# Optimization experiments

Hardware: AMD Instinct MI355X
Metric: run time of the kernel (lower is better)

The kernel has to match this reference:

```python
import jax, jax.numpy as jnp
import numpy as np

N = 4096
D = 256
TEMP = 0.1
NEG_INF = -1e30
NUM_IDS = 1000
NUM_CAMS = 8


def setup_inputs() -> dict:
    key = jax.random.key(0)
    k1, k2, k3 = jax.random.split(key, 3)
    features = jax.random.normal(k1, (N, 2, D), dtype=jnp.float32)
    label = jax.random.randint(k2, (N,), 0, NUM_IDS)
    camid = jax.random.randint(k3, (N,), 0, NUM_CAMS)
    return {"features": features, "label": label, "camid": camid}


def reference(features, label, camid):
    n = features.shape[0]
    n2 = 2 * n
    # torch.cat(torch.unbind(features, dim=1), dim=0): [N,2,D] -> [2N,D]
    f = jnp.concatenate([features[:, 0], features[:, 1]], axis=0)
    # pairwise similarity, pre-scaled by 1/temperature (original divides each
    # per-positive logit row by T, which is equivalent)
    logit = jnp.matmul(f, f.T) / TEMP  # [2N, 2N]
    diag = jnp.eye(n2, dtype=bool)
    lg = jnp.where(diag, NEG_INF, logit)  # diagonal excluded by masked_select
    m = jnp.max(lg, axis=1, keepdims=True)  # stable shift per row
    e = jnp.exp(lg - m)  # exp(logit - m), 0 on diagonal

    label_eq = label[:, None] == label[None, :]          # [N, N]
    cam_eq = camid[:, None] == camid[None, :]
    pos_id = jnp.tile(label_eq, (2, 2))                  # label_mask.repeat(2,2)
    pos_cam = jnp.tile(label_eq & cam_eq, (2, 2))        # is_pos.repeat(2,2)

    def branch(pos_full, row_scale):
        pm = pos_full & ~diag        # positives (off-diagonal)
        nm = ~pos_full               # negatives (diagonal is positive -> excluded)
        neg_sum = jnp.sum(jnp.where(nm, e, 0.0), axis=1, keepdims=True)
        # per-positive CE with label 0 over [positive, negatives]:
        #   log(exp(l_p - m) + neg_sum) + m - l_p
        per = jnp.log(jnp.where(pm, e + neg_sum, 1.0)) - (lg - m)
        num_pos = jnp.sum(pm, axis=1).astype(lg.dtype)
        row = jnp.sum(jnp.where(pm, per, 0.0), axis=1) / num_pos
        return row_scale * row

    loss_rows = branch(pos_id, 1.0) + branch(pos_cam, 0.5)
    loss = jnp.sum(loss_rows) / n2
    return loss
```

## Files before the change

kernel.cpp:

```cpp
#include <hip/hip_runtime.h>

typedef __attribute__((ext_vector_type(8))) _Float16 h8v;
typedef __attribute__((ext_vector_type(8))) short    s8v;
typedef __attribute__((ext_vector_type(4))) float    f4v;

#define N_   4096
#define N2   8192
#define D_   256
#define NIDS 1000
#define LCAP 32

constexpr float INV_TEMP = 10.0f;
constexpr float K_LOG2   = 14.426950408889634f;
constexpr float LN2F     = 0.6931471805599453f;
constexpr float NEGINF   = -1e30f;

__device__ __forceinline__ const float* frow(const float* f, int r) {
    return f + (size_t)(r & (N_ - 1)) * (2 * D_) + (size_t)((r >> 12) * D_);
}

__device__ __forceinline__ void gload_lds16(const void* g, void* l) {
    __builtin_amdgcn_global_load_lds(
        (const __attribute__((address_space(1))) void*)g,
        (__attribute__((address_space(3))) void*)l, 16, 0, 0);
}

__global__ __launch_bounds__(256) void prepK(const float* __restrict__ feat,
                                             const int* __restrict__ label,
                                             _Float16* __restrict__ f16,
                                             int* __restrict__ lists,
                                             int* __restrict__ done) {
    if (blockIdx.x < 1024) {
        int t = blockIdx.x * 256 + threadIdx.x;
        int r = t >> 5, g = t & 31;
        const float* src = frow(feat, r) + g * 8;
        float4 v0 = *(const float4*)src;
        float4 v1 = *(const float4*)(src + 4);
        float x[8] = {v0.x, v0.y, v0.z, v0.w, v1.x, v1.y, v1.z, v1.w};
        h8v h;
        #pragma unroll
        for (int i = 0; i < 8; ++i) h[i] = (_Float16)x[i];
        *(h8v*)(f16 + (size_t)r * D_ + g * 8) = h;
    } else {
        if (blockIdx.x == 1024 && threadIdx.x == 0) *done = 0;
        int cls  = (blockIdx.x - 1024) * 4 + (threadIdx.x >> 6);
        int lane = threadIdx.x & 63;
        int* Lp = lists + (size_t)cls * (LCAP + 1);
        int cnt = 0;
        for (int jj = 0; jj < N_; jj += 64) {
            unsigned long long mk = __ballot(label[jj + lane] == cls);
            while (mk) {
                int b = __ffsll((unsigned long long)mk) - 1;
                mk &= mk - 1;
                if (lane == 0 && cnt < LCAP) Lp[1 + cnt] = jj + b;
                ++cnt;
            }
        }
        if (lane == 0) Lp[0] = (cnt < LCAP) ? cnt : LCAP;
    }
}

__global__ __launch_bounds__(256, 4) void phaseA(const _Float16* __restrict__ f16,
                                                 const int* __restrict__ label,
                                                 float2* __restrict__ partial) {
    __shared__ char lds[32768];

    const int tid  = threadIdx.x;
    const int lane = tid & 63;
    const int w    = tid >> 6;
    const int wr   = w >> 1, wc = w & 1;

    int idx = (blockIdx.x & 7) * 260 + (blockIdx.x >> 3);
    int rt = 0, rem = idx;
    while (rem >= 64 - rt) { rem -= 64 - rt; ++rt; }
    const int ct = rt + rem;
    const bool offdiag = (ct != rt);
    const int rowBase = rt * 128, colBase = ct * 128;

    f4v acc[4][4];
    #pragma unroll
    for (int i = 0; i < 4; ++i)
        #pragma unroll
        for (int j = 0; j < 4; ++j) acc[i][j] = (f4v){0.f, 0.f, 0.f, 0.f};

    const int prB = (w < 2) ? rowBase : colBase;
    const int ssrc = (lane & 3) ^ ((lane >> 3) & 3);
    const _Float16* gl = f16 + (size_t)(prB + (w & 1) * 64 + (lane >> 2)) * D_ + ssrc * 8;
    const int ldoff = ((w >= 2) ? 8192 : 0) + (w & 1) * 4096 + lane * 16;

    #pragma unroll
    for (int i = 0; i < 4; ++i)
        gload_lds16(gl + (size_t)i * 16 * D_, lds + ldoff + i * 1024);
    __syncthreads();

    const int l15  = lane & 15;
    const int phys = ((lane >> 4) ^ ((l15 >> 1) & 3)) * 16;
    const int aoff0 = (wr * 64 + l15) * 64 + phys;
    const int boff0 = 8192 + (wc * 64 + l15) * 64 + phys;

    for (int kc = 0; kc < 8; ++kc) {
        const int cur = kc & 1;
        if (kc < 7) {
            const _Float16* gk = gl + (kc + 1) * 32;
            char* lp = lds + (cur ^ 1) * 16384 + ldoff;
            #pragma unroll
            for (int i = 0; i < 4; ++i)
                gload_lds16(gk + (size_t)i * 16 * D_, lp + i * 1024);
        }
        const char* bb = lds + cur * 16384;
        h8v a[4], b[4];
        #pragma unroll
        for (int rf = 0; rf < 4; ++rf) a[rf] = *(const h8v*)(bb + aoff0 + rf * 1024);
        #pragma unroll
        for (int cf = 0; cf < 4; ++cf) b[cf] = *(const h8v*)(bb + boff0 + cf * 1024);
        #pragma unroll
        for (int rf = 0; rf < 4; ++rf)
            #pragma unroll
            for (int cf = 0; cf < 4; ++cf)
                acc[rf][cf] = __builtin_amdgcn_mfma_f32_16x16x32_f16(a[rf], b[cf], acc[rf][cf], 0, 0, 0);
        __syncthreads();
    }

    float* rowm  = (float*)lds;
    float* colm  = (float*)(lds + 16896);
    float* mrowS = (float*)(lds + 21504);
    float* mcolS = (float*)(lds + 22016);

    const int grp32 = wc * 16 + l15;
    const int grp8  = wr * 4 + (lane >> 4);
    int rloc[16], cloc[4];
    int rowlab[16], collab[4];
    #pragma unroll
    for (int rf = 0; rf < 4; ++rf)
        #pragma unroll
        for (int rg = 0; rg < 4; ++rg) {
            int i = rf * 4 + rg;
            rloc[i] = wr * 64 + rf * 16 + (lane >> 4) * 4 + rg;
            rowlab[i] = label[(rowBase + rloc[i]) & (N_ - 1)];
        }
    #pragma unroll
    for (int cf = 0; cf < 4; ++cf) {
        cloc[cf] = wc * 64 + cf * 16 + l15;
        collab[cf] = label[(colBase + cloc[cf]) & (N_ - 1)];
    }

    #pragma unroll
    for (int rf = 0; rf < 4; ++rf)
        #pragma unroll
        for (int cf = 0; cf < 4; ++cf)
            #pragma unroll
            for (int rg = 0; rg < 4; ++rg) {
                float v = acc[rf][cf][rg] * K_LOG2;
                acc[rf][cf][rg] = (collab[cf] == rowlab[rf * 4 + rg]) ? NEGINF : v;
            }

    #pragma unroll
    for (int rf = 0; rf < 4; ++rf)
        #pragma unroll
        for (int rg = 0; rg < 4; ++rg) {
            float m = fmaxf(fmaxf(acc[rf][0][rg], acc[rf][1][rg]),
                            fmaxf(acc[rf][2][rg], acc[rf][3][rg]));
            rowm[rloc[rf * 4 + rg] * 33 + grp32] = m;
        }
    if (offdiag) {
        #pragma unroll
        for (int cf = 0; cf < 4; ++cf) {
            float m = NEGINF;
            #pragma unroll
            for (int rf = 0; rf < 4; ++rf)
                #pragma unroll
                for (int rg = 0; rg < 4; ++rg) m = fmaxf(m, acc[rf][cf][rg]);
            colm[cloc[cf] * 9 + grp8] = m;
        }
    }
    __syncthreads();
    if (tid < 128) {
        float m = NEGINF;
        #pragma unroll
        for (int g = 0; g < 32; ++g) m = fmaxf(m, rowm[tid * 33 + g]);
        mrowS[tid] = m;
        if (offdiag) {
            float mc = NEGINF;
            #pragma unroll
            for (int g = 0; g < 8; ++g) mc = fmaxf(mc, colm[tid * 9 + g]);
            mcolS[tid] = mc;
        }
    }
    __syncthreads();

    #pragma unroll
    for (int rf = 0; rf < 4; ++rf)
        #pragma unroll
        for (int rg = 0; rg < 4; ++rg) {
            int i = rf * 4 + rg;
            float m = mrowS[rloc[i]];
            float s = 0.f;
            #pragma unroll
            for (int cf = 0; cf < 4; ++cf) s += exp2f(acc[rf][cf][rg] - m);
            rowm[rloc[i] * 33 + grp32] = s;
        }
    if (offdiag) {
        #pragma unroll
        for (int cf = 0; cf < 4; ++cf) {
            float m = mcolS[cloc[cf]];
            float s = 0.f;
            #pragma unroll
            for (int rf = 0; rf < 4; ++rf)
                #pragma unroll
                for (int rg = 0; rg < 4; ++rg) s += exp2f(acc[rf][cf][rg] - m);
            colm[cloc[cf] * 9 + grp8] = s;
        }
    }
    __syncthreads();
    if (tid < 128) {
        float s = 0.f;
        #pragma unroll
        for (int g = 0; g < 32; ++g) s += rowm[tid * 33 + g];
        partial[(size_t)(rowBase + tid) * 64 + ct] = make_float2(mrowS[tid], s);
        if (offdiag) {
            float s2 = 0.f;
            #pragma unroll
            for (int g = 0; g < 8; ++g) s2 += colm[tid * 9 + g];
            partial[(size_t)(colBase + tid) * 64 + rt] = make_float2(mcolS[tid], s2);
        }
    }
}

__global__ __launch_bounds__(512) void phaseB(const float* __restrict__ feat,
                                              const int* __restrict__ label,
                                              const int* __restrict__ camid,
                                              const int* __restrict__ lists,
                                              const float2* __restrict__ partial,
                                              float* __restrict__ rowloss,
                                              int* __restrict__ done,
                                              float* __restrict__ out) {
    __shared__ int   cList[8][64];
    __shared__ int   fList[8][64];
    __shared__ float pList[8][64];
    __shared__ float red[512];
    __shared__ int   lastFlag;

    const int tid = threadIdx.x, lane = tid & 63, w = tid >> 6;
    const int row = blockIdx.x * 8 + w;
    const int rl = label[row & (N_ - 1)];
    const int rc = camid[row & (N_ - 1)];

    float2 p = partial[(size_t)row * 64 + lane];
    float mm = p.x, ms = p.y;
    #pragma unroll
    for (int off = 32; off >= 1; off >>= 1) {
        float om = __shfl_xor(mm, off), os = __shfl_xor(ms, off);
        float nm = fmaxf(mm, om);
        ms = ms * exp2f(mm - nm) + os * exp2f(om - nm);
        mm = nm;
    }
    const float cid = (mm + __log2f(ms)) * LN2F;

    const int li = lane & 15, g = lane >> 4;
    const float4* fip = (const float4*)frow(feat, row);
    float4 fiv[4];
    #pragma unroll
    for (int k = 0; k < 4; ++k) fiv[k] = fip[li * 4 + k];

    const int* Lp = lists + (size_t)rl * (LCAP + 1);
    const int nmem = Lp[0];
    int jm = (lane < 2 * nmem) ? Lp[1 + (lane >> 1)] : -1;
    int cand = jm + (lane & 1) * N_;
    bool valid = (jm >= 0) && (cand != row);
    unsigned long long mask = __ballot(valid);
    int cnt = __popcll(mask);
    int pos = __popcll(mask & ((1ull << lane) - 1ull));
    if (valid) {
        cList[w][pos] = cand;
        fList[w][pos] = (camid[jm] == rc) ? 1 : 0;
    }

    const int nb = (cnt + 3) >> 2;
    for (int b = 0; b < nb; ++b) {
        int e = b * 4 + g;
        bool act = (e < cnt);
        int c = act ? cList[w][e] : row;
        const float4* fcp = (const float4*)frow(feat, c);
        float pp = 0.f;
        #pragma unroll
        for (int k = 0; k < 4; ++k) {
            float4 v = fcp[li * 4 + k];
            pp += fiv[k].x * v.x + fiv[k].y * v.y + fiv[k].z * v.z + fiv[k].w * v.w;
        }
        #pragma unroll
        for (int off = 8; off >= 1; off >>= 1) pp += __shfl_xor(pp, off);
        if (act && li == 0) pList[w][e] = pp * INV_TEMP;
    }

    float a_e = (lane < cnt) ? pList[w][lane] : NEGINF;
    int   f_e = (lane < cnt) ? fList[w][lane] : 1;

    float xa = (f_e == 0) ? a_e : NEGINF;
    float mx = xa;
    #pragma unroll
    for (int off = 32; off >= 1; off >>= 1) mx = fmaxf(mx, __shfl_xor(mx, off));
    float xe = (f_e == 0) ? __expf(xa - mx) : 0.f;
    #pragma unroll
    for (int off = 32; off >= 1; off >>= 1) xe += __shfl_xor(xe, off);
    float ccam;
    if (xe > 0.f) {
        float xl = mx + __logf(xe);
        float d = xl - cid;
        ccam = (d <= 0.f) ? cid + log1pf(__expf(d)) : xl + log1pf(__expf(-d));
    } else {
        ccam = cid;
    }

    float ti = cid - a_e;
    float termid = (ti <= 0.f) ? log1pf(__expf(ti)) : ti + log1pf(__expf(-ti));
    termid = (lane < cnt) ? termid : 0.f;
    float tc = ccam - a_e;
    float termcam = (tc <= 0.f) ? log1pf(__expf(tc)) : tc + log1pf(__expf(-tc));
    termcam = (lane < cnt && f_e) ? termcam : 0.f;
    #pragma unroll
    for (int off = 32; off >= 1; off >>= 1) {
        termid  += __shfl_xor(termid, off);
        termcam += __shfl_xor(termcam, off);
    }
    int ncam = __popcll(__ballot(lane < cnt && f_e));
    if (lane == 0)
        rowloss[row] = termid / (float)cnt + 0.5f * termcam / (float)ncam;

    __syncthreads();
    if (tid == 0) {
        __threadfence();
        lastFlag = (atomicAdd(done, 1) == (int)gridDim.x - 1) ? 1 : 0;
    }
    __syncthreads();
    if (lastFlag) {
        __threadfence();
        float s = 0.f;
        const int b0 = tid * 16;
        #pragma unroll
        for (int i = 0; i < 16; ++i) s += rowloss[b0 + i];
        red[tid] = s;
        __syncthreads();
        for (int ww = 256; ww > 0; ww >>= 1) {
            if (tid < ww) red[tid] += red[tid + ww];
            __syncthreads();
        }
        if (tid == 0) out[0] = red[0] / (float)N2;
    }
}

extern "C" void kernel_launch(void* const* d_in, const int* in_sizes, int n_in,
                              void* d_out, int out_size, void* d_ws, size_t ws_size,
                              hipStream_t stream) {
    const float* feat  = (const float*)d_in[0];
    const int*   label = (const int*)d_in[1];
    const int*   camid = (const int*)d_in[2];

    _Float16* f16    = (_Float16*)d_ws;
    float2*   partial = (float2*)((char*)d_ws + 4u * 1024 * 1024);
    float*    rowloss = (float*)((char*)d_ws + 8u * 1024 * 1024);
    int*      lists   = (int*)(rowloss + N2);
    int*      done    = lists + NIDS * (LCAP + 1);

    prepK<<<1274, 256, 0, stream>>>(feat, label, f16, lists, done);
    phaseA<<<2080, 256, 0, stream>>>(f16, label, partial);
    phaseB<<<1024, 512, 0, stream>>>(feat, label, camid, lists, partial,
                                     rowloss, done, (float*)d_out);
}
```

Measured before the change: 95.60 us.

## Fuse GEMM and per-row loss phases into one persistent kernel with spin-wait

Merges phaseA (tiled fp16 MFMA Gram matrix with masked log-sum-exp partials) and phaseB (per-row positive dot products and loss) into one launch. The trailing blocks first build each row's same-label candidate list by scanning all labels, which replaces the per-class list pass in prepK, then spin on an atomic counter until every GEMM tile has finished. The tile order is reversed through a closed-form triangular index, and each loss block now handles 32 rows. This removes one kernel launch boundary and overlaps candidate discovery with the GEMM. In exchange it depends on all GEMM blocks being scheduled ahead of the spinning blocks, and each loss block does a much larger label scan.

```diff
diff --git a/kernel.cpp b/kernel.cpp
--- a/kernel.cpp
+++ b/kernel.cpp
@@ -1,14 +1,13 @@
 #include <hip/hip_runtime.h>
 
 typedef __attribute__((ext_vector_type(8))) _Float16 h8v;
-typedef __attribute__((ext_vector_type(8))) short    s8v;
 typedef __attribute__((ext_vector_type(4))) float    f4v;
 
-#define N_   4096
-#define N2   8192
-#define D_   256
-#define NIDS 1000
-#define LCAP 32
+#define N_     4096
+#define N2     8192
+#define D_     256
+#define ATILES 2080
+#define BBLK   256
 
 constexpr float INV_TEMP = 10.0f;
 constexpr float K_LOG2   = 14.426950408889634f;
@@ -26,321 +25,346 @@
 }
 
 __global__ __launch_bounds__(256) void prepK(const float* __restrict__ feat,
-                                             const int* __restrict__ label,
                                              _Float16* __restrict__ f16,
-                                             int* __restrict__ lists,
                                              int* __restrict__ done) {
-    if (blockIdx.x < 1024) {
-        int t = blockIdx.x * 256 + threadIdx.x;
-        int r = t >> 5, g = t & 31;
-        const float* src = frow(feat, r) + g * 8;
-        float4 v0 = *(const float4*)src;
-        float4 v1 = *(const float4*)(src + 4);
-        float x[8] = {v0.x, v0.y, v0.z, v0.w, v1.x, v1.y, v1.z, v1.w};
-        h8v h;
-        #pragma unroll
-        for (int i = 0; i < 8; ++i) h[i] = (_Float16)x[i];
-        *(h8v*)(f16 + (size_t)r * D_ + g * 8) = h;
-    } else {
-        if (blockIdx.x == 1024 && threadIdx.x == 0) *done = 0;
-        int cls  = (blockIdx.x - 1024) * 4 + (threadIdx.x >> 6);
-        int lane = threadIdx.x & 63;
-        int* Lp = lists + (size_t)cls * (LCAP + 1);
-        int cnt = 0;
-        for (int jj = 0; jj < N_; jj += 64) {
-            unsigned long long mk = __ballot(label[jj + lane] == cls);
+    if (blockIdx.x == 0 && threadIdx.x == 0) { done[0] = 0; done[1] = 0; }
+    int t = blockIdx.x * 256 + threadIdx.x;
+    int r = t >> 5, g = t & 31;
+    const float* src = frow(feat, r) + g * 8;
+    float4 v0 = *(const float4*)src;
+    float4 v1 = *(const float4*)(src + 4);
+    float x[8] = {v0.x, v0.y, v0.z, v0.w, v1.x, v1.y, v1.z, v1.w};
+    h8v h;
+    #pragma unroll
+    for (int i = 0; i < 8; ++i) h[i] = (_Float16)x[i];
+    *(h8v*)(f16 + (size_t)r * D_ + g * 8) = h;
+}
+
+__global__ __launch_bounds__(256, 4) void mega(const _Float16* __restrict__ f16,
+                                               const float* __restrict__ feat,
+                                               const int* __restrict__ label,
+                                               const int* __restrict__ camid,
+                                               float2* __restrict__ partial,
+                                               float* __restrict__ rowloss,
+                                               int* __restrict__ done,
+                                               float* __restrict__ out) {
+    __shared__ char lds[32768];
+    const int tid  = threadIdx.x;
+    const int lane = tid & 63;
+    const int w    = tid >> 6;
+
+    if (blockIdx.x < ATILES) {
+        const int wr = w >> 1, wc = w & 1;
+        int idx = (blockIdx.x & 7) * 260 + (blockIdx.x >> 3);
+        int rev = 2079 - idx;
+        int r2 = (int)((sqrtf((float)(8 * rev + 1)) - 1.0f) * 0.5f);
+        if (r2 * (r2 + 1) / 2 > rev) --r2;
+        else if ((r2 + 1) * (r2 + 2) / 2 <= rev) ++r2;
+        const int rt = 63 - r2;
+        const int ct = 63 - (rev - r2 * (r2 + 1) / 2);
+        const bool offdiag = (ct != rt);
+        const int rowBase = rt * 128, colBase = ct * 128;
+
+        f4v acc[4][4];
+        #pragma unroll
+        for (int i = 0; i < 4; ++i)
+            #pragma unroll
+            for (int j = 0; j < 4; ++j) acc[i][j] = (f4v){0.f, 0.f, 0.f, 0.f};
+
+        const int prB = (w < 2) ? rowBase : colBase;
+        const int ssrc = (lane & 3) ^ ((lane >> 3) & 3);
+        const _Float16* gl = f16 + (size_t)(prB + (w & 1) * 64 + (lane >> 2)) * D_ + ssrc * 8;
+        const int ldoff = ((w >= 2) ? 8192 : 0) + (w & 1) * 4096 + lane * 16;
+
+        #pragma unroll
+        for (int i = 0; i < 4; ++i)
+            gload_lds16(gl + (size_t)i * 16 * D_, lds + ldoff + i * 1024);
+        __syncthreads();
+
+        const int l15  = lane & 15;
+        const int phys = ((lane >> 4) ^ ((l15 >> 1) & 3)) * 16;
+        const int aoff0 = (wr * 64 + l15) * 64 + phys;
+        const int boff0 = 8192 + (wc * 64 + l15) * 64 + phys;
+
+        for (int kc = 0; kc < 8; ++kc) {
+            const int cur = kc & 1;
+            if (kc < 7) {
+                const _Float16* gk = gl + (kc + 1) * 32;
+                char* lp = lds + (cur ^ 1) * 16384 + ldoff;
+                #pragma unroll
+                for (int i = 0; i < 4; ++i)
+                    gload_lds16(gk + (size_t)i * 16 * D_, lp + i * 1024);
+            }
+            const char* bb = lds + cur * 16384;
+            h8v a[4], b[4];
+            #pragma unroll
+            for (int rf = 0; rf < 4; ++rf) a[rf] = *(const h8v*)(bb + aoff0 + rf * 1024);
+            #pragma unroll
+            for (int cf = 0; cf < 4; ++cf) b[cf] = *(const h8v*)(bb + boff0 + cf * 1024);
+            #pragma unroll
+            for (int rf = 0; rf < 4; ++rf)
+                #pragma unroll
+                for (int cf = 0; cf < 4; ++cf)
+                    acc[rf][cf] = __builtin_amdgcn_mfma_f32_16x16x32_f16(a[rf], b[cf], acc[rf][cf], 0, 0, 0);
+            __syncthreads();
+        }
+
+        float* rowm  = (float*)lds;
+        float* colm  = (float*)(lds + 16896);
+        float* mrowS = (float*)(lds + 21504);
+        float* mcolS = (float*)(lds + 22016);
+
+        const int grp32 = wc * 16 + l15;
+        const int grp8  = wr * 4 + (lane >> 4);
+        int rloc[16], cloc[4], rowlab[16], collab[4];
+        #pragma unroll
+        for (int rf = 0; rf < 4; ++rf)
+            #pragma unroll
+            for (int rg = 0; rg < 4; ++rg) {
+                int i = rf * 4 + rg;
+                rloc[i] = wr * 64 + rf * 16 + (lane >> 4) * 4 + rg;
+                rowlab[i] = label[(rowBase + rloc[i]) & (N_ - 1)];
+            }
+        #pragma unroll
+        for (int cf = 0; cf < 4; ++cf) {
+            cloc[cf] = wc * 64 + cf * 16 + l15;
+            collab[cf] = label[(colBase + cloc[cf]) & (N_ - 1)];
+        }
+
+        #pragma unroll
+        for (int rf = 0; rf < 4; ++rf)
+            #pragma unroll
+            for (int cf = 0; cf < 4; ++cf)
+                #pragma unroll
+                for (int rg = 0; rg < 4; ++rg) {
+                    float v = acc[rf][cf][rg] * K_LOG2;
+                    acc[rf][cf][rg] = (collab[cf] == rowlab[rf * 4 + rg]) ? NEGINF : v;
+                }
+
+        #pragma unroll
+        for (int rf = 0; rf < 4; ++rf)
+            #pragma unroll
+            for (int rg = 0; rg < 4; ++rg) {
+                float m = fmaxf(fmaxf(acc[rf][0][rg], acc[rf][1][rg]),
+                                fmaxf(acc[rf][2][rg], acc[rf][3][rg]));
+                rowm[rloc[rf * 4 + rg] * 33 + grp32] = m;
+            }
+        if (offdiag) {
+            #pragma unroll
+            for (int cf = 0; cf < 4; ++cf) {
+                float m = NEGINF;
+                #pragma unroll
+                for (int rf = 0; rf < 4; ++rf)
+                    #pragma unroll
+                    for (int rg = 0; rg < 4; ++rg) m = fmaxf(m, acc[rf][cf][rg]);
+                colm[cloc[cf] * 9 + grp8] = m;
+            }
+        }
+        __syncthreads();
+        if (tid < 128) {
+            float m = NEGINF;
+            #pragma unroll
+            for (int g = 0; g < 32; ++g) m = fmaxf(m, rowm[tid * 33 + g]);
+            mrowS[tid] = m;
+            if (offdiag) {
+                float mc = NEGINF;
+                #pragma unroll
+                for (int g = 0; g < 8; ++g) mc = fmaxf(mc, colm[tid * 9 + g]);
+                mcolS[tid] = mc;
+            }
+        }
+        __syncthreads();
+
+        #pragma unroll
+        for (int rf = 0; rf < 4; ++rf)
+            #pragma unroll
+            for (int rg = 0; rg < 4; ++rg) {
+                int i = rf * 4 + rg;
+                float m = mrowS[rloc[i]];
+                float s = 0.f;
+                #pragma unroll
+                for (int cf = 0; cf < 4; ++cf) s += exp2f(acc[rf][cf][rg] - m);
+                rowm[rloc[i] * 33 + grp32] = s;
+            }
+        if (offdiag) {
+            #pragma unroll
+            for (int cf = 0; cf < 4; ++cf) {
+                float m = mcolS[cloc[cf]];
+                float s = 0.f;
+                #pragma unroll
+                for (int rf = 0; rf < 4; ++rf)
+                    #pragma unroll
+                    for (int rg = 0; rg < 4; ++rg) s += exp2f(acc[rf][cf][rg] - m);
+                colm[cloc[cf] * 9 + grp8] = s;
+            }
+        }
+        __syncthreads();
+        if (tid < 128) {
+            float s = 0.f;
+            #pragma unroll
+            for (int g = 0; g < 32; ++g) s += rowm[tid * 33 + g];
+            partial[(size_t)(rowBase + tid) * 64 + ct] = make_float2(mrowS[tid], s);
+            if (offdiag) {
+                float s2 = 0.f;
+                #pragma unroll
+                for (int g = 0; g < 8; ++g) s2 += colm[tid * 9 + g];
+                partial[(size_t)(colBase + tid) * 64 + rt] = make_float2(mcolS[tid], s2);
+            }
+        }
+        __syncthreads();
+        if (tid == 0) {
+            __threadfence();
+            atomicAdd(&done[0], 1);
+        }
+        return;
+    }
+
+    int*   candN = (int*)lds;
+    int*   candJ = (int*)(lds + 128);
+    int*   cList = (int*)(lds + 4224);
+    float* pList = (float*)(lds + 5248);
+    float* red   = (float*)(lds + 6272);
+    int*   lastF = (int*)(lds + 7296);
+
+    const int r0 = (blockIdx.x - ATILES) * 32 + w * 8;
+
+    int rl[8], rc[8], nq[8];
+    #pragma unroll
+    for (int q = 0; q < 8; ++q) {
+        int m = (r0 + q) & (N_ - 1);
+        rl[q] = label[m];
+        rc[q] = camid[m];
+        nq[q] = 0;
+    }
+    for (int jj = 0; jj < N_; jj += 64) {
+        int lj = label[jj + lane], cj = camid[jj + lane];
+        #pragma unroll
+        for (int q = 0; q < 8; ++q) {
+            unsigned long long mk = __ballot(lj == rl[q]);
             while (mk) {
                 int b = __ffsll((unsigned long long)mk) - 1;
                 mk &= mk - 1;
-                if (lane == 0 && cnt < LCAP) Lp[1 + cnt] = jj + b;
-                ++cnt;
-            }
-        }
-        if (lane == 0) Lp[0] = (cnt < LCAP) ? cnt : LCAP;
-    }
-}
-
-__global__ __launch_bounds__(256, 4) void phaseA(const _Float16* __restrict__ f16,
-                                                 const int* __restrict__ label,
-                                                 float2* __restrict__ partial) {
-    __shared__ char lds[32768];
-
-    const int tid  = threadIdx.x;
-    const int lane = tid & 63;
-    const int w    = tid >> 6;
-    const int wr   = w >> 1, wc = w & 1;
-
-    int idx = (blockIdx.x & 7) * 260 + (blockIdx.x >> 3);
-    int rt = 0, rem = idx;
-    while (rem >= 64 - rt) { rem -= 64 - rt; ++rt; }
-    const int ct = rt + rem;
-    const bool offdiag = (ct != rt);
-    const int rowBase = rt * 128, colBase = ct * 128;
-
-    f4v acc[4][4];
+                int cm = (__shfl(cj, b) == rc[q]) ? 1 : 0;
+                if (lane == 0 && nq[q] < 32)
+                    candJ[(w * 8 + q) * 32 + nq[q]] = (jj + b) | (cm << 30);
+                ++nq[q];
+            }
+        }
+    }
     #pragma unroll
-    for (int i = 0; i < 4; ++i)
-        #pragma unroll
-        for (int j = 0; j < 4; ++j) acc[i][j] = (f4v){0.f, 0.f, 0.f, 0.f};
-
-    const int prB = (w < 2) ? rowBase : colBase;
-    const int ssrc = (lane & 3) ^ ((lane >> 3) & 3);
-    const _Float16* gl = f16 + (size_t)(prB + (w & 1) * 64 + (lane >> 2)) * D_ + ssrc * 8;
-    const int ldoff = ((w >= 2) ? 8192 : 0) + (w & 1) * 4096 + lane * 16;
-
-    #pragma unroll
-    for (int i = 0; i < 4; ++i)
-        gload_lds16(gl + (size_t)i * 16 * D_, lds + ldoff + i * 1024);
+    for (int q = 0; q < 8; ++q)
+        if (lane == 0) candN[w * 8 + q] = (nq[q] < 32) ? nq[q] : 32;
     __syncthreads();
 
-    const int l15  = lane & 15;
-    const int phys = ((lane >> 4) ^ ((l15 >> 1) & 3)) * 16;
-    const int aoff0 = (wr * 64 + l15) * 64 + phys;
-    const int boff0 = 8192 + (wc * 64 + l15) * 64 + phys;
-
-    for (int kc = 0; kc < 8; ++kc) {
-        const int cur = kc & 1;
-        if (kc < 7) {
-            const _Float16* gk = gl + (kc + 1) * 32;
-            char* lp = lds + (cur ^ 1) * 16384 + ldoff;
-            #pragma unroll
-            for (int i = 0; i < 4; ++i)
-                gload_lds16(gk + (size_t)i * 16 * D_, lp + i * 1024);
-        }
-        const char* bb = lds + cur * 16384;
-        h8v a[4], b[4];
-        #pragma unroll
-        for (int rf = 0; rf < 4; ++rf) a[rf] = *(const h8v*)(bb + aoff0 + rf * 1024);
-        #pragma unroll
-        for (int cf = 0; cf < 4; ++cf) b[cf] = *(const h8v*)(bb + boff0 + cf * 1024);
-        #pragma unroll
-        for (int rf = 0; rf < 4; ++rf)
-            #pragma unroll
-            for (int cf = 0; cf < 4; ++cf)
-                acc[rf][cf] = __builtin_amdgcn_mfma_f32_16x16x32_f16(a[rf], b[cf], acc[rf][cf], 0, 0, 0);
-        __syncthreads();
-    }
-
-    float* rowm  = (float*)lds;
-    float* colm  = (float*)(lds + 16896);
-    float* mrowS = (float*)(lds + 21504);
-    float* mcolS = (float*)(lds + 22016);
-
-    const int grp32 = wc * 16 + l15;
-    const int grp8  = wr * 4 + (lane >> 4);
-    int rloc[16], cloc[4];
-    int rowlab[16], collab[4];
-    #pragma unroll
-    for (int rf = 0; rf < 4; ++rf)
-        #pragma unroll
-        for (int rg = 0; rg < 4; ++rg) {
-            int i = rf * 4 + rg;
-            rloc[i] = wr * 64 + rf * 16 + (lane >> 4) * 4 + rg;
-            rowlab[i] = label[(rowBase + rloc[i]) & (N_ - 1)];
-        }
-    #pragma unroll
-    for (int cf = 0; cf < 4; ++cf) {
-        cloc[cf] = wc * 64 + cf * 16 + l15;
-        collab[cf] = label[(colBase + cloc[cf]) & (N_ - 1)];
-    }
-
-    #pragma unroll
-    for (int rf = 0; rf < 4; ++rf)
-        #pragma unroll
-        for (int cf = 0; cf < 4; ++cf)
-            #pragma unroll
-            for (int rg = 0; rg < 4; ++rg) {
-                float v = acc[rf][cf][rg] * K_LOG2;
-                acc[rf][cf][rg] = (collab[cf] == rowlab[rf * 4 + rg]) ? NEGINF : v;
-            }
-
-    #pragma unroll
-    for (int rf = 0; rf < 4; ++rf)
-        #pragma unroll
-        for (int rg = 0; rg < 4; ++rg) {
-            float m = fmaxf(fmaxf(acc[rf][0][rg], acc[rf][1][rg]),
-                            fmaxf(acc[rf][2][rg], acc[rf][3][rg]));
-            rowm[rloc[rf * 4 + rg] * 33 + grp32] = m;
-        }
-    if (offdiag) {
-        #pragma unroll
-        for (int cf = 0; cf < 4; ++cf) {
-            float m = NEGINF;
-            #pragma unroll
-            for (int rf = 0; rf < 4; ++rf)
-                #pragma unroll
-                for (int rg = 0; rg < 4; ++rg) m = fmaxf(m, acc[rf][cf][rg]);
-            colm[cloc[cf] * 9 + grp8] = m;
-        }
+    if (tid == 0) {
+        while (__hip_atomic_load(&done[0], __ATOMIC_ACQUIRE, __HIP_MEMORY_SCOPE_AGENT) < ATILES)
+            __builtin_amdgcn_s_sleep(16);
     }
     __syncthreads();
-    if (tid < 128) {
-        float m = NEGINF;
-        #pragma unroll
-        for (int g = 0; g < 32; ++g) m = fmaxf(m, rowm[tid * 33 + g]);
-        mrowS[tid] = m;
-        if (offdiag) {
-            float mc = NEGINF;
-            #pragma unroll
-            for (int g = 0; g < 8; ++g) mc = fmaxf(mc, colm[tid * 9 + g]);
-            mcolS[tid] = mc;
-        }
-    }
-    __syncthreads();
-
-    #pragma unroll
-    for (int rf = 0; rf < 4; ++rf)
-        #pragma unroll
-        for (int rg = 0; rg < 4; ++rg) {
-            int i = rf * 4 + rg;
-            float m = mrowS[rloc[i]];
-            float s = 0.f;
-            #pragma unroll
-            for (int cf = 0; cf < 4; ++cf) s += exp2f(acc[rf][cf][rg] - m);
-            rowm[rloc[i] * 33 + grp32] = s;
-        }
-    if (offdiag) {
-        #pragma unroll
-        for (int cf = 0; cf < 4; ++cf) {
-            float m = mcolS[cloc[cf]];
-            float s = 0.f;
-            #pragma unroll
-            for (int rf = 0; rf < 4; ++rf)
-                #pragma unroll
-                for (int rg = 0; rg < 4; ++rg) s += exp2f(acc[rf][cf][rg] - m);
-            colm[cloc[cf] * 9 + grp8] = s;
-        }
-    }
-    __syncthreads();
-    if (tid < 128) {
-        float s = 0.f;
-        #pragma unroll
-        for (int g = 0; g < 32; ++g) s += rowm[tid * 33 + g];
-        partial[(size_t)(rowBase + tid) * 64 + ct] = make_float2(mrowS[tid], s);
-        if (offdiag) {
-            float s2 = 0.f;
-            #pragma unroll
-            for (int g = 0; g < 8; ++g) s2 += colm[tid * 9 + g];
-            partial[(size_t)(colBase + tid) * 64 + rt] = make_float2(mcolS[tid], s2);
-        }
-    }
-}
-
-__global__ __launch_bounds__(512) void phaseB(const float* __restrict__ feat,
-                                              const int* __restrict__ label,
-                                              const int* __restrict__ camid,
-                                              const int* __restrict__ lists,
-                                              const float2* __restrict__ partial,
-                                              float* __restrict__ rowloss,
-                                              int* __restrict__ done,
-                                              float* __restrict__ out) {
-    __shared__ int   cList[8][64];
-    __shared__ int   fList[8][64];
-    __shared__ float pList[8][64];
-    __shared__ float red[512];
-    __shared__ int   lastFlag;
-
-    const int tid = threadIdx.x, lane = tid & 63, w = tid >> 6;
-    const int row = blockIdx.x * 8 + w;
-    const int rl = label[row & (N_ - 1)];
-    const int rc = camid[row & (N_ - 1)];
-
-    float2 p = partial[(size_t)row * 64 + lane];
-    float mm = p.x, ms = p.y;
-    #pragma unroll
-    for (int off = 32; off >= 1; off >>= 1) {
-        float om = __shfl_xor(mm, off), os = __shfl_xor(ms, off);
-        float nm = fmaxf(mm, om);
-        ms = ms * exp2f(mm - nm) + os * exp2f(om - nm);
-        mm = nm;
-    }
-    const float cid = (mm + __log2f(ms)) * LN2F;
+    __threadfence();
 
     const int li = lane & 15, g = lane >> 4;
-    const float4* fip = (const float4*)frow(feat, row);
-    float4 fiv[4];
-    #pragma unroll
-    for (int k = 0; k < 4; ++k) fiv[k] = fip[li * 4 + k];
-
-    const int* Lp = lists + (size_t)rl * (LCAP + 1);
-    const int nmem = Lp[0];
-    int jm = (lane < 2 * nmem) ? Lp[1 + (lane >> 1)] : -1;
-    int cand = jm + (lane & 1) * N_;
-    bool valid = (jm >= 0) && (cand != row);
-    unsigned long long mask = __ballot(valid);
-    int cnt = __popcll(mask);
-    int pos = __popcll(mask & ((1ull << lane) - 1ull));
-    if (valid) {
-        cList[w][pos] = cand;
-        fList[w][pos] = (camid[jm] == rc) ? 1 : 0;
-    }
-
-    const int nb = (cnt + 3) >> 2;
-    for (int b = 0; b < nb; ++b) {
-        int e = b * 4 + g;
-        bool act = (e < cnt);
-        int c = act ? cList[w][e] : row;
-        const float4* fcp = (const float4*)frow(feat, c);
-        float pp = 0.f;
-        #pragma unroll
-        for (int k = 0; k < 4; ++k) {
-            float4 v = fcp[li * 4 + k];
-            pp += fiv[k].x * v.x + fiv[k].y * v.y + fiv[k].z * v.z + fiv[k].w * v.w;
-        }
-        #pragma unroll
-        for (int off = 8; off >= 1; off >>= 1) pp += __shfl_xor(pp, off);
-        if (act && li == 0) pList[w][e] = pp * INV_TEMP;
-    }
-
-    float a_e = (lane < cnt) ? pList[w][lane] : NEGINF;
-    int   f_e = (lane < cnt) ? fList[w][lane] : 1;
-
-    float xa = (f_e == 0) ? a_e : NEGINF;
-    float mx = xa;
-    #pragma unroll
-    for (int off = 32; off >= 1; off >>= 1) mx = fmaxf(mx, __shfl_xor(mx, off));
-    float xe = (f_e == 0) ? __expf(xa - mx) : 0.f;
-    #pragma unroll
-    for (int off = 32; off >= 1; off >>= 1) xe += __shfl_xor(xe, off);
-    float ccam;
-    if (xe > 0.f) {
-        float xl = mx + __logf(xe);
-        float d = xl - cid;
-        ccam = (d <= 0.f) ? cid + log1pf(__expf(d)) : xl + log1pf(__expf(-d));
-    } else {
-        ccam = cid;
-    }
-
-    float ti = cid - a_e;
-    float termid = (ti <= 0.f) ? log1pf(__expf(ti)) : ti + log1pf(__expf(-ti));
-    termid = (lane < cnt) ? termid : 0.f;
-    float tc = ccam - a_e;
-    float termcam = (tc <= 0.f) ? log1pf(__expf(tc)) : tc + log1pf(__expf(-tc));
-    termcam = (lane < cnt && f_e) ? termcam : 0.f;
-    #pragma unroll
-    for (int off = 32; off >= 1; off >>= 1) {
-        termid  += __shfl_xor(termid, off);
-        termcam += __shfl_xor(termcam, off);
-    }
-    int ncam = __popcll(__ballot(lane < cnt && f_e));
-    if (lane == 0)
-        rowloss[row] = termid / (float)cnt + 0.5f * termcam / (float)ncam;
+
+    #pragma unroll 1
+    for (int q = 0; q < 8; ++q) {
+        const int row = r0 + q;
+        const int rcq = camid[row & (N_ - 1)];
+
+        float2 p = partial[(size_t)row * 64 + lane];
+        float mm = p.x, ms = p.y;
+        #pragma unroll
+        for (int off = 32; off >= 1; off >>= 1) {
+            float om = __shfl_xor(mm, off), os = __shfl_xor(ms, off);
+            float nm = fmaxf(mm, om);
+            ms = ms * exp2f(mm - nm) + os * exp2f(om - nm);
+            mm = nm;
+        }
+        const float cid = (mm + __log2f(ms)) * LN2F;
+
+        float4 fiv[4];
+        const float4* fip = (const float4*)frow(feat, row);
+        #pragma unroll
+        for (int k = 0; k < 4; ++k) fiv[k] = fip[li * 4 + k];
+
+        const int n = candN[w * 8 + q];
+        int jm = (lane < 2 * n) ? candJ[(w * 8 + q) * 32 + (lane >> 1)] : -1;
+        int cand = (jm & 0xFFFF) + (lane & 1) * N_;
+        bool valid = (jm >= 0) && (cand != row);
+        unsigned long long mask = __ballot(valid);
+        int cnt = __popcll(mask);
+        int pos = __popcll(mask & ((1ull << lane) - 1ull));
+        if (valid) cList[w * 64 + pos] = cand | (jm & (1 << 30));
+
+        const int nb = (cnt + 3) >> 2;
+        for (int b = 0; b < nb; ++b) {
+            int e = b * 4 + g;
+            bool act = (e < cnt);
+            int c = act ? (cList[w * 64 + e] & 0xFFFF) : row;
+            const float4* fcp = (const float4*)frow(feat, c);
+            float pp = 0.f;
+            #pragma unroll
+            for (int k = 0; k < 4; ++k) {
+                float4 v = fcp[li * 4 + k];
+                pp += fiv[k].x * v.x + fiv[k].y * v.y + fiv[k].z * v.z + fiv[k].w * v.w;
+            }
+            #pragma unroll
+            for (int off = 8; off >= 1; off >>= 1) pp += __shfl_xor(pp, off);
+            if (act && li == 0) pList[w * 64 + e] = pp * INV_TEMP;
+        }
+
+        int ce   = (lane < cnt) ? cList[w * 64 + lane] : -1;
+        float a_e = (lane < cnt) ? pList[w * 64 + lane] : NEGINF;
+        int   f_e = (lane < cnt) ? ((ce >> 30) & 1) : 1;
+
+        float xa = (f_e == 0) ? a_e : NEGINF;
+        float mx = xa;
+        #pragma unroll
+        for (int off = 32; off >= 1; off >>= 1) mx = fmaxf(mx, __shfl_xor(mx, off));
+        float xe = (f_e == 0) ? __expf(xa - mx) : 0.f;
+        #pragma unroll
+        for (int off = 32; off >= 1; off >>= 1) xe += __shfl_xor(xe, off);
+        float ccam;
+        if (xe > 0.f) {
+            float xl = mx + __logf(xe);
+            float d = xl - cid;
+            ccam = (d <= 0.f) ? cid + log1pf(__expf(d)) : xl + log1pf(__expf(-d));
+        } else {
+            ccam = cid;
+        }
+
+        float ti = cid - a_e;
+        float termid = (ti <= 0.f) ? log1pf(__expf(ti)) : ti + log1pf(__expf(-ti));
+        termid = (lane < cnt) ? termid : 0.f;
+        float tc = ccam - a_e;
+        float termcam = (tc <= 0.f) ? log1pf(__expf(tc)) : tc + log1pf(__expf(-tc));
+        termcam = (lane < cnt && f_e) ? termcam : 0.f;
+        #pragma unroll
+        for (int off = 32; off >= 1; off >>= 1) {
+            termid  += __shfl_xor(termid, off);
+            termcam += __shfl_xor(termcam, off);
+        }
+        int ncam = __popcll(__ballot(lane < cnt && f_e));
+        if (lane == 0)
+            rowloss[row] = termid / (float)cnt + 0.5f * termcam / (float)ncam;
+
+        __builtin_amdgcn_wave_barrier();
+    }
 
     __syncthreads();
     if (tid == 0) {
         __threadfence();
-        lastFlag = (atomicAdd(done, 1) == (int)gridDim.x - 1) ? 1 : 0;
+        *lastF = (atomicAdd(&done[1], 1) == BBLK - 1) ? 1 : 0;
     }
     __syncthreads();
-    if (lastFlag) {
+    if (*lastF) {
         __threadfence();
         float s = 0.f;
-        const int b0 = tid * 16;
-        #pragma unroll
-        for (int i = 0; i < 16; ++i) s += rowloss[b0 + i];
+        const int b0 = tid * 32;
+        #pragma unroll
+        for (int i = 0; i < 32; ++i) s += rowloss[b0 + i];
         red[tid] = s;
         __syncthreads();
-        for (int ww = 256; ww > 0; ww >>= 1) {
+        for (int ww = 128; ww > 0; ww >>= 1) {
             if (tid < ww) red[tid] += red[tid + ww];
             __syncthreads();
         }
@@ -355,14 +379,12 @@
     const int*   label = (const int*)d_in[1];
     const int*   camid = (const int*)d_in[2];
 
-    _Float16* f16    = (_Float16*)d_ws;
+    _Float16* f16     = (_Float16*)d_ws;
     float2*   partial = (float2*)((char*)d_ws + 4u * 1024 * 1024);
     float*    rowloss = (float*)((char*)d_ws + 8u * 1024 * 1024);
-    int*      lists   = (int*)(rowloss + N2);
-    int*      done    = lists + NIDS * (LCAP + 1);
-
-    prepK<<<1274, 256, 0, stream>>>(feat, label, f16, lists, done);
-    phaseA<<<2080, 256, 0, stream>>>(f16, label, partial);
-    phaseB<<<1024, 512, 0, stream>>>(feat, label, camid, lists, partial,
-                                     rowloss, done, (float*)d_out);
-}
+    int*      done    = (int*)(rowloss + N2);
+
+    prepK<<<1024, 256, 0, stream>>>(feat, f16, done);
+    mega<<<ATILES + BBLK, 256, 0, stream>>>(f16, feat, label, camid, partial,
+                                            rowloss, done, (float*)d_out);
+}
```

Result: slower. 200.1 us (+109.3%).

## Reuse phaseA positive-pair logits instead of recomputing dot products in phaseB

Applied to the files above, without the earlier changes.

PhaseA now writes the logits of same-label pairs into a per-row scatter buffer, indexed through a new per-sample slot map built in prepK. PhaseB reads these instead of reloading fp32 feature rows and redoing the dot products, so its block size and grid change. The 1/T and log2 scaling is folded into the fp16 conversion by multiplying features by sqrt(K), which removes the per-element multiply in the epilogue. In exchange phaseA gets extra scattered global stores, an added barrier and a higher occupancy hint. Positive logits now come from fp16 MFMA rather than fp32, which costs some precision.

```diff
diff --git a/kernel.cpp b/kernel.cpp
--- a/kernel.cpp
+++ b/kernel.cpp
@@ -1,7 +1,6 @@
 #include <hip/hip_runtime.h>
 
 typedef __attribute__((ext_vector_type(8))) _Float16 h8v;
-typedef __attribute__((ext_vector_type(8))) short    s8v;
 typedef __attribute__((ext_vector_type(4))) float    f4v;
 
 #define N_   4096
@@ -10,10 +9,9 @@
 #define NIDS 1000
 #define LCAP 32
 
-constexpr float INV_TEMP = 10.0f;
-constexpr float K_LOG2   = 14.426950408889634f;
-constexpr float LN2F     = 0.6931471805599453f;
-constexpr float NEGINF   = -1e30f;
+constexpr float LN2F   = 0.6931471805599453f;
+constexpr float NEGINF = -1e30f;
+constexpr float SQRT_K = 3.7982826f;
 
 __device__ __forceinline__ const float* frow(const float* f, int r) {
     return f + (size_t)(r & (N_ - 1)) * (2 * D_) + (size_t)((r >> 12) * D_);
@@ -29,8 +27,10 @@
                                              const int* __restrict__ label,
                                              _Float16* __restrict__ f16,
                                              int* __restrict__ lists,
+                                             int* __restrict__ idxmap,
                                              int* __restrict__ done) {
     if (blockIdx.x < 1024) {
+        if (blockIdx.x == 0 && threadIdx.x == 0) *done = 0;
         int t = blockIdx.x * 256 + threadIdx.x;
         int r = t >> 5, g = t & 31;
         const float* src = frow(feat, r) + g * 8;
@@ -39,10 +39,9 @@
         float x[8] = {v0.x, v0.y, v0.z, v0.w, v1.x, v1.y, v1.z, v1.w};
         h8v h;
         #pragma unroll
-        for (int i = 0; i < 8; ++i) h[i] = (_Float16)x[i];
+        for (int i = 0; i < 8; ++i) h[i] = (_Float16)(x[i] * SQRT_K);
         *(h8v*)(f16 + (size_t)r * D_ + g * 8) = h;
     } else {
-        if (blockIdx.x == 1024 && threadIdx.x == 0) *done = 0;
         int cls  = (blockIdx.x - 1024) * 4 + (threadIdx.x >> 6);
         int lane = threadIdx.x & 63;
         int* Lp = lists + (size_t)cls * (LCAP + 1);
@@ -52,7 +51,10 @@
             while (mk) {
                 int b = __ffsll((unsigned long long)mk) - 1;
                 mk &= mk - 1;
-                if (lane == 0 && cnt < LCAP) Lp[1 + cnt] = jj + b;
+                if (lane == 0 && cnt < LCAP) {
+                    Lp[1 + cnt] = jj + b;
+                    idxmap[jj + b] = cnt;
+                }
                 ++cnt;
             }
         }
@@ -60,9 +62,11 @@
     }
 }
 
-__global__ __launch_bounds__(256, 4) void phaseA(const _Float16* __restrict__ f16,
+__global__ __launch_bounds__(256, 5) void phaseA(const _Float16* __restrict__ f16,
                                                  const int* __restrict__ label,
-                                                 float2* __restrict__ partial) {
+                                                 const int* __restrict__ idxmap,
+                                                 float2* __restrict__ partial,
+                                                 float* __restrict__ plog) {
     __shared__ char lds[32768];
 
     const int tid  = threadIdx.x;
@@ -121,15 +125,21 @@
         __syncthreads();
     }
 
-    float* rowm  = (float*)lds;
-    float* colm  = (float*)(lds + 16896);
-    float* mrowS = (float*)(lds + 21504);
-    float* mcolS = (float*)(lds + 22016);
+    float* rowm    = (float*)lds;
+    float* colm    = (float*)(lds + 16896);
+    float* mrowS   = (float*)(lds + 21504);
+    float* mcolS   = (float*)(lds + 22016);
+    int*   rowIdxS = (int*)(lds + 22528);
+    int*   colIdxS = (int*)(lds + 23040);
+
+    if (tid < 128) {
+        rowIdxS[tid] = idxmap[(rowBase + tid) & (N_ - 1)];
+        colIdxS[tid] = idxmap[(colBase + tid) & (N_ - 1)];
+    }
 
     const int grp32 = wc * 16 + l15;
     const int grp8  = wr * 4 + (lane >> 4);
-    int rloc[16], cloc[4];
-    int rowlab[16], collab[4];
+    int rloc[16], cloc[4], rowlab[16], collab[4];
     #pragma unroll
     for (int rf = 0; rf < 4; ++rf)
         #pragma unroll
@@ -143,6 +153,7 @@
         cloc[cf] = wc * 64 + cf * 16 + l15;
         collab[cf] = label[(colBase + cloc[cf]) & (N_ - 1)];
     }
+    __syncthreads();
 
     #pragma unroll
     for (int rf = 0; rf < 4; ++rf)
@@ -150,8 +161,17 @@
         for (int cf = 0; cf < 4; ++cf)
             #pragma unroll
             for (int rg = 0; rg < 4; ++rg) {
-                float v = acc[rf][cf][rg] * K_LOG2;
-                acc[rf][cf][rg] = (collab[cf] == rowlab[rf * 4 + rg]) ? NEGINF : v;
+                int i = rf * 4 + rg;
+                float v = acc[rf][cf][rg];
+                bool match = (collab[cf] == rowlab[i]);
+                if (match) {
+                    int gr = rowBase + rloc[i], gc = colBase + cloc[cf];
+                    if (gc > gr) {
+                        plog[(size_t)gr * 64 + ((colIdxS[cloc[cf]] * 2 + (gc >> 12)) & 63)] = v;
+                        plog[(size_t)gc * 64 + ((rowIdxS[rloc[i]] * 2 + (gr >> 12)) & 63)] = v;
+                    }
+                }
+                acc[rf][cf][rg] = match ? NEGINF : v;
             }
 
     #pragma unroll
@@ -226,22 +246,19 @@
     }
 }
 
-__global__ __launch_bounds__(512) void phaseB(const float* __restrict__ feat,
-                                              const int* __restrict__ label,
+__global__ __launch_bounds__(256) void phaseB(const int* __restrict__ label,
                                               const int* __restrict__ camid,
                                               const int* __restrict__ lists,
                                               const float2* __restrict__ partial,
+                                              const float* __restrict__ plog,
                                               float* __restrict__ rowloss,
                                               int* __restrict__ done,
                                               float* __restrict__ out) {
-    __shared__ int   cList[8][64];
-    __shared__ int   fList[8][64];
-    __shared__ float pList[8][64];
-    __shared__ float red[512];
-    __shared__ int   lastFlag;
+    __shared__ float red[256];
+    __shared__ int lastF;
 
     const int tid = threadIdx.x, lane = tid & 63, w = tid >> 6;
-    const int row = blockIdx.x * 8 + w;
+    const int row = blockIdx.x * 4 + w;
     const int rl = label[row & (N_ - 1)];
     const int rc = camid[row & (N_ - 1)];
 
@@ -256,50 +273,21 @@
     }
     const float cid = (mm + __log2f(ms)) * LN2F;
 
-    const int li = lane & 15, g = lane >> 4;
-    const float4* fip = (const float4*)frow(feat, row);
-    float4 fiv[4];
-    #pragma unroll
-    for (int k = 0; k < 4; ++k) fiv[k] = fip[li * 4 + k];
-
     const int* Lp = lists + (size_t)rl * (LCAP + 1);
     const int nmem = Lp[0];
-    int jm = (lane < 2 * nmem) ? Lp[1 + (lane >> 1)] : -1;
-    int cand = jm + (lane & 1) * N_;
-    bool valid = (jm >= 0) && (cand != row);
-    unsigned long long mask = __ballot(valid);
-    int cnt = __popcll(mask);
-    int pos = __popcll(mask & ((1ull << lane) - 1ull));
-    if (valid) {
-        cList[w][pos] = cand;
-        fList[w][pos] = (camid[jm] == rc) ? 1 : 0;
-    }
-
-    const int nb = (cnt + 3) >> 2;
-    for (int b = 0; b < nb; ++b) {
-        int e = b * 4 + g;
-        bool act = (e < cnt);
-        int c = act ? cList[w][e] : row;
-        const float4* fcp = (const float4*)frow(feat, c);
-        float pp = 0.f;
-        #pragma unroll
-        for (int k = 0; k < 4; ++k) {
-            float4 v = fcp[li * 4 + k];
-            pp += fiv[k].x * v.x + fiv[k].y * v.y + fiv[k].z * v.z + fiv[k].w * v.w;
-        }
-        #pragma unroll
-        for (int off = 8; off >= 1; off >>= 1) pp += __shfl_xor(pp, off);
-        if (act && li == 0) pList[w][e] = pp * INV_TEMP;
-    }
-
-    float a_e = (lane < cnt) ? pList[w][lane] : NEGINF;
-    int   f_e = (lane < cnt) ? fList[w][lane] : 1;
-
-    float xa = (f_e == 0) ? a_e : NEGINF;
+    int member = (lane < 2 * nmem) ? Lp[1 + (lane >> 1)] : -1;
+    int cand = member + (lane & 1) * N_;
+    bool valid = (member >= 0) && (cand != row);
+    float a_e = valid ? plog[(size_t)row * 64 + lane] * LN2F : NEGINF;
+    int f_e = valid ? ((camid[member] == rc) ? 1 : 0) : 1;
+
+    int cnt = __popcll(__ballot(valid));
+
+    float xa = (valid && !f_e) ? a_e : NEGINF;
     float mx = xa;
     #pragma unroll
     for (int off = 32; off >= 1; off >>= 1) mx = fmaxf(mx, __shfl_xor(mx, off));
-    float xe = (f_e == 0) ? __expf(xa - mx) : 0.f;
+    float xe = (valid && !f_e) ? __expf(xa - mx) : 0.f;
     #pragma unroll
     for (int off = 32; off >= 1; off >>= 1) xe += __shfl_xor(xe, off);
     float ccam;
@@ -313,34 +301,34 @@
 
     float ti = cid - a_e;
     float termid = (ti <= 0.f) ? log1pf(__expf(ti)) : ti + log1pf(__expf(-ti));
-    termid = (lane < cnt) ? termid : 0.f;
+    termid = valid ? termid : 0.f;
     float tc = ccam - a_e;
     float termcam = (tc <= 0.f) ? log1pf(__expf(tc)) : tc + log1pf(__expf(-tc));
-    termcam = (lane < cnt && f_e) ? termcam : 0.f;
+    termcam = (valid && f_e) ? termcam : 0.f;
     #pragma unroll
     for (int off = 32; off >= 1; off >>= 1) {
         termid  += __shfl_xor(termid, off);
         termcam += __shfl_xor(termcam, off);
     }
-    int ncam = __popcll(__ballot(lane < cnt && f_e));
+    int ncam = __popcll(__ballot(valid && f_e));
     if (lane == 0)
         rowloss[row] = termid / (float)cnt + 0.5f * termcam / (float)ncam;
 
     __syncthreads();
     if (tid == 0) {
         __threadfence();
-        lastFlag = (atomicAdd(done, 1) == (int)gridDim.x - 1) ? 1 : 0;
-    }
-    __syncthreads();
-    if (lastFlag) {
+        lastF = (atomicAdd(done, 1) == (int)gridDim.x - 1) ? 1 : 0;
+    }
+    __syncthreads();
+    if (lastF) {
         __threadfence();
         float s = 0.f;
-        const int b0 = tid * 16;
-        #pragma unroll
-        for (int i = 0; i < 16; ++i) s += rowloss[b0 + i];
+        const int b0 = tid * 32;
+        #pragma unroll
+        for (int i = 0; i < 32; ++i) s += rowloss[b0 + i];
         red[tid] = s;
         __syncthreads();
-        for (int ww = 256; ww > 0; ww >>= 1) {
+        for (int ww = 128; ww > 0; ww >>= 1) {
             if (tid < ww) red[tid] += red[tid + ww];
             __syncthreads();
         }
@@ -355,14 +343,16 @@
     const int*   label = (const int*)d_in[1];
     const int*   camid = (const int*)d_in[2];
 
-    _Float16* f16    = (_Float16*)d_ws;
+    _Float16* f16     = (_Float16*)d_ws;
     float2*   partial = (float2*)((char*)d_ws + 4u * 1024 * 1024);
-    float*    rowloss = (float*)((char*)d_ws + 8u * 1024 * 1024);
+    float*    plog    = (float*)((char*)d_ws + 8u * 1024 * 1024);
+    float*    rowloss = (float*)((char*)d_ws + 10u * 1024 * 1024);
     int*      lists   = (int*)(rowloss + N2);
-    int*      done    = lists + NIDS * (LCAP + 1);
-
-    prepK<<<1274, 256, 0, stream>>>(feat, label, f16, lists, done);
-    phaseA<<<2080, 256, 0, stream>>>(f16, label, partial);
-    phaseB<<<1024, 512, 0, stream>>>(feat, label, camid, lists, partial,
+    int*      idxmap  = lists + NIDS * (LCAP + 1);
+    int*      done    = idxmap + N_;
+
+    prepK<<<1274, 256, 0, stream>>>(feat, label, f16, lists, idxmap, done);
+    phaseA<<<2080, 256, 0, stream>>>(f16, label, idxmap, partial, plog);
+    phaseB<<<2048, 256, 0, stream>>>(label, camid, lists, partial, plog,
                                      rowloss, done, (float*)d_out);
 }
```

After: 131.8 us. 37.9% more time.
